# Kernel tuning notes

Hardware: AMD Instinct MI355X
Metric: run time of the kernel (lower is better)

## Reference

```python
import jax, jax.numpy as jnp
import numpy as np

N = 16384
E = 524288
K = 16
IN_C, HID, OUT = 3, 64, 64


def _mlp(h, Wa, ba, Wb, bb):
    # Linear -> ReLU -> Linear -> ReLU (as in nn.Sequential)
    return jax.nn.relu(jax.nn.relu(h @ Wa + ba) @ Wb + bb)


def _edgeconv(x, src, dst, Wa, ba, Wb, bb, n):
    # PyG EdgeConv message: nn([x_i, x_j - x_i]) with i=dst (target), j=src (source)
    xi = x[dst]                       # [E, C]
    xj = x[src]                       # [E, C]
    m = _mlp(jnp.concatenate([xi, xj - xi], axis=-1), Wa, ba, Wb, bb)  # [E, H]
    out = jax.ops.segment_max(m, dst, num_segments=n)
    # nodes with no incoming edges: fill 0 (PyG scatter-max fill value)
    return jnp.where(jnp.isfinite(out), out, 0.0)


def _knn_edges(x, k):
    # pairwise squared distances in feature space; includes self (torch_cluster.knn(x, x, k))
    sq = jnp.sum(x * x, axis=1)                      # [N]
    dist = sq[:, None] + sq[None, :] - 2.0 * (x @ x.T)  # [N, N]
    _, idx = jax.lax.top_k(-dist, k)                 # [N, k] nearest (incl. self)
    src = idx.reshape(-1)
    dst = jnp.repeat(jnp.arange(x.shape[0]), k)
    return src, dst


def setup_inputs() -> dict:
    key = jax.random.key(0)
    ks = jax.random.split(key, 8)
    sc = lambda fan: 1.0 / np.sqrt(fan)
    return {
        "x": jax.random.normal(ks[0], (N, IN_C), dtype=jnp.float32),
        "edge_index": jax.random.randint(ks[1], (2, E), 0, N, dtype=jnp.int64),
        "k": K,
        "W1": jax.random.normal(ks[2], (2 * IN_C, HID), dtype=jnp.float32) * sc(2 * IN_C),
        "b1": jnp.zeros((HID,), dtype=jnp.float32),
        "W2": jax.random.normal(ks[3], (HID, HID), dtype=jnp.float32) * sc(HID),
        "b2": jnp.zeros((HID,), dtype=jnp.float32),
        "W3": jax.random.normal(ks[4], (2 * HID, OUT), dtype=jnp.float32) * sc(2 * HID),
        "b3": jnp.zeros((OUT,), dtype=jnp.float32),
        "W4": jax.random.normal(ks[5], (OUT, OUT), dtype=jnp.float32) * sc(OUT),
        "b4": jnp.zeros((OUT,), dtype=jnp.float32),
    }


def reference(x, edge_index, k, W1, b1, W2, b2, W3, b3, W4, b4):
    n = x.shape[0]
    # static EdgeConv (edge_index[0]=source j, edge_index[1]=target i)
    x1 = _edgeconv(x, edge_index[0], edge_index[1], W1, b1, W2, b2, n)
    # DynamicEdgeConv: kNN in feature space of x1, then EdgeConv
    src2, dst2 = _knn_edges(x1, k)
    x2 = _edgeconv(x1, src2, dst2, W3, b3, W4, b4, n)
    return x2
```

## Files before the change

kernel.cpp:

```cpp
#include <hip/hip_runtime.h>
#include <stdint.h>

#define NN   16384
#define NE   524288
#define TK   17
#define TAU  4e-5f

#define S1   2048
#define JC1  16
#define CH1  (S1 / JC1)
#define JCB  8
#define CAP  512
#define LCAP 64
#define OFB  256
#define MGNB2 1e-3f

typedef unsigned long long u64;
typedef unsigned int u32;
typedef unsigned short u16;
typedef __attribute__((ext_vector_type(8))) short bf16x8;
typedef __attribute__((ext_vector_type(4))) float f32x4;

__device__ __forceinline__ float mulrn(float a, float b) { return __fmul_rn(a, b); }
__device__ __forceinline__ float addrn(float a, float b) { return __fadd_rn(a, b); }
__device__ __forceinline__ float subrn(float a, float b) { return __fsub_rn(a, b); }

__device__ __forceinline__ u32 fkey(float f) {
    u32 b = __float_as_uint(f);
    return ((int)b < 0) ? ~b : (b | 0x80000000u);
}
__device__ __forceinline__ float inv_fkey(u32 k) {
    return (k & 0x80000000u) ? __uint_as_float(k & 0x7fffffffu) : __uint_as_float(~k);
}

__device__ __forceinline__ u16 f2bf(float f) {
    u32 x = __float_as_uint(f);
    u32 r = x + 0x7fffu + ((x >> 16) & 1u);
    return (u16)(r >> 16);
}

template<int K>
__device__ __forceinline__ void topk_insert(u64 (&key)[K], u64 nk) {
#pragma unroll
    for (int s = K - 1; s >= 1; --s) {
        bool c1 = nk < key[s - 1];
        bool c0 = nk < key[s];
        key[s] = c1 ? key[s - 1] : (c0 ? nk : key[s]);
    }
    if (nk < key[0]) key[0] = nk;
}

#define XR_DECL float4 xq0, xq1, xq2, xq3, xq4, xq5, xq6, xq7, \
                       xq8, xq9, xq10, xq11, xq12, xq13, xq14, xq15

#define XR_LOAD(ptr) do { const float4* xp_ = (const float4*)(ptr); \
    xq0  = xp_[0];  xq1  = xp_[1];  xq2  = xp_[2];  xq3  = xp_[3]; \
    xq4  = xp_[4];  xq5  = xp_[5];  xq6  = xp_[6];  xq7  = xp_[7]; \
    xq8  = xp_[8];  xq9  = xp_[9];  xq10 = xp_[10]; xq11 = xp_[11]; \
    xq12 = xp_[12]; xq13 = xp_[13]; xq14 = xp_[14]; xq15 = xp_[15]; } while (0)

#define DOT_STEP(res, qq, w_) \
    res = fmaf(qq.x, w_.x, res); res = fmaf(qq.y, w_.y, res); \
    res = fmaf(qq.z, w_.z, res); res = fmaf(qq.w, w_.w, res);

#define DOT64(res, ptr) do { const float4* jp_ = (const float4*)(ptr); \
    float4 w_ = jp_[0]; \
    res = mulrn(xq0.x, w_.x); res = fmaf(xq0.y, w_.y, res); \
    res = fmaf(xq0.z, w_.z, res); res = fmaf(xq0.w, w_.w, res); \
    w_ = jp_[1];  DOT_STEP(res, xq1,  w_) \
    w_ = jp_[2];  DOT_STEP(res, xq2,  w_) \
    w_ = jp_[3];  DOT_STEP(res, xq3,  w_) \
    w_ = jp_[4];  DOT_STEP(res, xq4,  w_) \
    w_ = jp_[5];  DOT_STEP(res, xq5,  w_) \
    w_ = jp_[6];  DOT_STEP(res, xq6,  w_) \
    w_ = jp_[7];  DOT_STEP(res, xq7,  w_) \
    w_ = jp_[8];  DOT_STEP(res, xq8,  w_) \
    w_ = jp_[9];  DOT_STEP(res, xq9,  w_) \
    w_ = jp_[10]; DOT_STEP(res, xq10, w_) \
    w_ = jp_[11]; DOT_STEP(res, xq11, w_) \
    w_ = jp_[12]; DOT_STEP(res, xq12, w_) \
    w_ = jp_[13]; DOT_STEP(res, xq13, w_) \
    w_ = jp_[14]; DOT_STEP(res, xq14, w_) \
    w_ = jp_[15]; DOT_STEP(res, xq15, w_) } while (0)

__global__ __launch_bounds__(256) void hist_kernel(const int* __restrict__ ei,
                                                   int* __restrict__ hist) {
    int e = blockIdx.x * 256 + threadIdx.x;
    atomicAdd(&hist[ei[NE + e]], 1);
}

__global__ __launch_bounds__(256) void scan_kernel(const int* __restrict__ hist,
                                                   int* __restrict__ base) {
    __shared__ int part[256];
    __shared__ int off[256];
    int t = threadIdx.x;
    int s = 0;
    for (int b = 0; b < 64; b++) s += hist[t * 64 + b];
    part[t] = s;
    __syncthreads();
    if (t == 0) {
        int run = 0;
        for (int i = 0; i < 256; i++) { off[i] = run; run += part[i]; }
    }
    __syncthreads();
    int run = off[t];
    for (int b = 0; b < 64; b++) {
        base[t * 64 + b] = run;
        run += hist[t * 64 + b];
    }
}

__global__ __launch_bounds__(256) void scatter_kernel(const int* __restrict__ ei,
                                                      int* __restrict__ base,
                                                      int* __restrict__ esrc,
                                                      int* __restrict__ edst) {
    int e = blockIdx.x * 256 + threadIdx.x;
    int d = ei[NE + e];
    int pos = atomicAdd(&base[d], 1);
    esrc[pos] = ei[e];
    edst[pos] = d;
}

__global__ __launch_bounds__(256) void conv1_np_kernel(const float* __restrict__ x,
                                                       const float* __restrict__ W1,
                                                       const float* __restrict__ b1,
                                                       const float* __restrict__ W2,
                                                       const float* __restrict__ b2,
                                                       const int* __restrict__ esrc,
                                                       const int* __restrict__ edst,
                                                       float* __restrict__ x1n) {
    __shared__ float HT[64 * 132];
    __shared__ float W1s[384];
    __shared__ float W2s[64 * 64];
    __shared__ float b1s[64], b2s[64];
    __shared__ int dsts[128];
    int t = threadIdx.x;
    int eb = blockIdx.x * 128;

    {
        const float4* w4 = (const float4*)W2;
        float4* wd = (float4*)W2s;
#pragma unroll
        for (int q = 0; q < 4; q++) wd[t + q * 256] = w4[t + q * 256];
        if (t < 96) ((float4*)W1s)[t] = ((const float4*)W1)[t];
        if (t < 64) { b1s[t] = b1[t]; b2s[t] = b2[t]; }
    }
    __syncthreads();

    {
        int el = t >> 1;
        int cb = (t & 1) * 32;
        int e = eb + el;
        int j = esrc[e];
        int i = edst[e];
        if ((t & 1) == 0) dsts[el] = i;
        float xi0 = x[i * 3 + 0], xi1 = x[i * 3 + 1], xi2 = x[i * 3 + 2];
        float xj0 = x[j * 3 + 0], xj1 = x[j * 3 + 1], xj2 = x[j * 3 + 2];
        float d0 = subrn(xj0, xi0), d1 = subrn(xj1, xi1), d2 = subrn(xj2, xi2);
#pragma unroll
        for (int cc = 0; cc < 32; cc++) {
            int c = cb + cc;
            float acc = mulrn(xi0, W1s[c]);
            acc = fmaf(xi1, W1s[64 + c], acc);
            acc = fmaf(xi2, W1s[128 + c], acc);
            acc = fmaf(d0,  W1s[192 + c], acc);
            acc = fmaf(d1,  W1s[256 + c], acc);
            acc = fmaf(d2,  W1s[320 + c], acc);
            HT[c * 132 + el] = fmaxf(addrn(acc, b1s[c]), 0.f);
        }
    }
    __syncthreads();

    int cg = t & 7, eg = t >> 3;
    int c0 = cg * 8, e0 = eg * 4;
    float acc[4][8] = {};
    for (int k = 0; k < 64; k++) {
        float4 a  = *(const float4*)&HT[k * 132 + e0];
        float4 w0 = *(const float4*)&W2s[k * 64 + c0];
        float4 w1 = *(const float4*)&W2s[k * 64 + c0 + 4];
        float av[4] = {a.x, a.y, a.z, a.w};
        float wv[8] = {w0.x, w0.y, w0.z, w0.w, w1.x, w1.y, w1.z, w1.w};
#pragma unroll
        for (int r = 0; r < 4; r++)
#pragma unroll
            for (int c = 0; c < 8; c++) acc[r][c] = fmaf(av[r], wv[c], acc[r][c]);
    }
    __syncthreads();
#pragma unroll
    for (int r = 0; r < 4; r++)
#pragma unroll
        for (int c = 0; c < 8; c++)
            HT[(c0 + c) * 132 + (e0 + r)] = fmaxf(addrn(acc[r][c], b2s[c0 + c]), 0.f);
    __syncthreads();

    {
        int col = t & 63;
        int ebeg = (t >> 6) * 32;
        const float* hp = &HT[col * 132];
        int cur = dsts[ebeg];
        float m = hp[ebeg];
        for (int e = ebeg + 1; e < ebeg + 32; e++) {
            int d2 = dsts[e];
            float v = hp[e];
            if (d2 == cur) {
                m = fmaxf(m, v);
            } else {
                atomicMax((u32*)(x1n + (size_t)cur * 64 + col), __float_as_uint(m));
                cur = d2;
                m = v;
            }
        }
        atomicMax((u32*)(x1n + (size_t)cur * 64 + col), __float_as_uint(m));
    }
}

__global__ __launch_bounds__(256) void sq_np_kernel(const float* __restrict__ x1,
                                                    float* __restrict__ sq) {
    int i = blockIdx.x * 256 + threadIdx.x;
    const float* p = x1 + (size_t)i * 64;
    float r[8];
#pragma unroll
    for (int j = 0; j < 8; j++) { float v = p[j]; r[j] = mulrn(v, v); }
#pragma unroll
    for (int b = 8; b < 64; b += 8)
#pragma unroll
        for (int j = 0; j < 8; j++) { float v = p[b + j]; r[j] = addrn(r[j], mulrn(v, v)); }
    sq[i] = addrn(addrn(addrn(r[0], r[1]), addrn(r[2], r[3])),
                  addrn(addrn(r[4], r[5]), addrn(r[6], r[7])));
}

__global__ __launch_bounds__(256) void cvt_bf_kernel(const float* __restrict__ x1,
                                                     u16* __restrict__ xb,
                                                     u16* __restrict__ xl) {
    int i = (blockIdx.x * 256 + threadIdx.x) * 8;
    uint4 oh, ol;
    u32 hw[8], lw[8];
#pragma unroll
    for (int q = 0; q < 8; q++) {
        float v = x1[i + q];
        u16 h = f2bf(v);
        float hf = __uint_as_float((u32)h << 16);
        u16 l = f2bf(subrn(v, hf));
        hw[q] = h; lw[q] = l;
    }
    oh.x = hw[0] | (hw[1] << 16); oh.y = hw[2] | (hw[3] << 16);
    oh.z = hw[4] | (hw[5] << 16); oh.w = hw[6] | (hw[7] << 16);
    ol.x = lw[0] | (lw[1] << 16); ol.y = lw[2] | (lw[3] << 16);
    ol.z = lw[4] | (lw[5] << 16); ol.w = lw[6] | (lw[7] << 16);
    *(uint4*)(xb + i) = oh;
    *(uint4*)(xl + i) = ol;
}

__global__ __launch_bounds__(256, 4) void knn_tau_kernel(const float* __restrict__ x1,
                                                         const float* __restrict__ sq,
                                                         u32* __restrict__ part1) {
    int rb = blockIdx.x >> 4;
    int ch = blockIdx.x & 15;
    int t = threadIdx.x;
    int r = rb * 256 + t;
    XR_DECL;
    XR_LOAD(x1 + (size_t)r * 64);
    float sqr = sq[r];
    u32 key[TK];
#pragma unroll
    for (int s = 0; s < TK; s++) key[s] = 0xFFFFFFFFu;
    int j0 = ch * CH1;
    for (int jj = 0; jj < CH1; jj++) {
        int j = j0 + jj;
        float a;
        DOT64(a, x1 + (size_t)j * 64);
        float dd = subrn(addrn(sqr, sq[j]), mulrn(2.f, a));
        u32 nk = fkey(dd);
#pragma unroll
        for (int s = TK - 1; s >= 1; --s) key[s] = min(max(nk, key[s - 1]), key[s]);
        key[0] = min(key[0], nk);
    }
    u32* pp = part1 + ((size_t)r * JC1 + ch) * TK;
#pragma unroll
    for (int s = 0; s < TK; s++) pp[s] = key[s];
}

__global__ __launch_bounds__(256) void tau_merge_kernel(const u32* __restrict__ part1,
                                                        float* __restrict__ tauf) {
    int r = blockIdx.x * 256 + threadIdx.x;
    u32 key[TK];
#pragma unroll
    for (int s = 0; s < TK; s++) key[s] = 0xFFFFFFFFu;
    const u32* cp = part1 + (size_t)r * (JC1 * TK);
    for (int c = 0; c < JC1; c++) {
        for (int s = 0; s < TK; s++) {
            u32 nk = cp[c * TK + s];
            if (nk >= key[TK - 1]) break;
#pragma unroll
            for (int q = TK - 1; q >= 1; --q) key[q] = min(max(nk, key[q - 1]), key[q]);
            key[0] = min(key[0], nk);
        }
    }
    tauf[r] = inv_fkey(key[TK - 1]);
}

__global__ __launch_bounds__(256, 3) void knn_collect_mfma(const u16* __restrict__ xb,
                                                           const u16* __restrict__ xl,
                                                           const float* __restrict__ sq,
                                                           const float* __restrict__ tauf,
                                                           int* __restrict__ ccnt,
                                                           u16* __restrict__ cidx) {
    __shared__ u16 slist[64 * LCAP];
    __shared__ int scnt[64];
    __shared__ int sbase[64];
    int rb = blockIdx.x >> 3;
    int jc = blockIdx.x & 7;
    int t = threadIdx.x;
    int w = t >> 6, l = t & 63;
    int lr = l & 15, lg = l >> 4;
    int rbase = rb * 64;
    if (t < 64) scnt[t] = 0;

    bf16x8 fah[4][2], fal[4][2];
#pragma unroll
    for (int rs = 0; rs < 4; rs++) {
        size_t off = (size_t)(rbase + rs * 16 + lr) * 64 + lg * 8;
        fah[rs][0] = *(const bf16x8*)(xb + off);
        fah[rs][1] = *(const bf16x8*)(xb + off + 32);
        fal[rs][0] = *(const bf16x8*)(xl + off);
        fal[rs][1] = *(const bf16x8*)(xl + off + 32);
    }
    float sqr[16], taur[16];
#pragma unroll
    for (int rs = 0; rs < 4; rs++)
#pragma unroll
        for (int i = 0; i < 4; i++) {
            int rr = rbase + rs * 16 + lg * 4 + i;
            sqr[rs * 4 + i]  = sq[rr];
            taur[rs * 4 + i] = tauf[rr];
        }
    __syncthreads();

    int j0 = jc * (NN / JCB) + w * (NN / JCB / 4);
    for (int js = 0; js < (NN / JCB / 4); js += 16) {
        int jb = j0 + js;
        size_t boff = (size_t)(jb + lr) * 64 + lg * 8;
        bf16x8 fbh0 = *(const bf16x8*)(xb + boff);
        bf16x8 fbh1 = *(const bf16x8*)(xb + boff + 32);
        bf16x8 fbl0 = *(const bf16x8*)(xl + boff);
        bf16x8 fbl1 = *(const bf16x8*)(xl + boff + 32);
        int j = jb + lr;
        float sqj = sq[j];
#pragma unroll
        for (int rs = 0; rs < 4; rs++) {
            f32x4 acc = {0.f, 0.f, 0.f, 0.f};
            acc = __builtin_amdgcn_mfma_f32_16x16x32_bf16(fah[rs][0], fbh0, acc, 0, 0, 0);
            acc = __builtin_amdgcn_mfma_f32_16x16x32_bf16(fah[rs][1], fbh1, acc, 0, 0, 0);
            acc = __builtin_amdgcn_mfma_f32_16x16x32_bf16(fah[rs][0], fbl0, acc, 0, 0, 0);
            acc = __builtin_amdgcn_mfma_f32_16x16x32_bf16(fah[rs][1], fbl1, acc, 0, 0, 0);
            acc = __builtin_amdgcn_mfma_f32_16x16x32_bf16(fal[rs][0], fbh0, acc, 0, 0, 0);
            acc = __builtin_amdgcn_mfma_f32_16x16x32_bf16(fal[rs][1], fbh1, acc, 0, 0, 0);
#pragma unroll
            for (int i = 0; i < 4; i++) {
                float ss = sqr[rs * 4 + i] + sqj;
                float dd = ss - 2.f * acc[i];
                if (dd <= taur[rs * 4 + i] + MGNB2 * ss) {
                    int rl = rs * 16 + lg * 4 + i;
                    int slot = atomicAdd(&scnt[rl], 1);
                    if (slot < LCAP) {
                        slist[rl * LCAP + slot] = (u16)j;
                    } else {
                        int rr = rbase + rl;
                        int gslot = atomicAdd(&ccnt[rr], 1);
                        if (gslot < CAP) cidx[(size_t)rr * CAP + gslot] = (u16)j;
                    }
                }
            }
        }
    }
    __syncthreads();

    if (t < 64) {
        int ldsn = min(scnt[t], LCAP);
        sbase[t] = (ldsn > 0) ? atomicAdd(&ccnt[rbase + t], ldsn) : -1;
    }
    __syncthreads();
    {
        int rl = t >> 2, ln = t & 3;
        int ldsn = min(scnt[rl], LCAP);
        int base = sbase[rl];
        if (base >= 0) {
            for (int s = ln; s < ldsn; s += 4) {
                int dst = base + s;
                if (dst < CAP)
                    cidx[(size_t)(rbase + rl) * CAP + dst] = slist[rl * LCAP + s];
            }
        }
    }
}

__global__ __launch_bounds__(256) void oflow_scan_kernel(const int* __restrict__ ccnt,
                                                         int* __restrict__ ocnt,
                                                         int* __restrict__ olist) {
    int r = blockIdx.x * 256 + threadIdx.x;
    if (ccnt[r] > CAP) {
        int s = atomicAdd(ocnt, 1);
        olist[s] = r;
    }
}

__global__ __launch_bounds__(256, 2) void oflow_fix_kernel(const float* __restrict__ x1,
                                                           const float* __restrict__ sq,
                                                           const int* __restrict__ ocnt,
                                                           const int* __restrict__ olist,
                                                           u16* __restrict__ cidx,
                                                           int* __restrict__ ccnt) {
    __shared__ u64 m[256 * TK];
    int nof = *ocnt;
    int t = threadIdx.x;
    for (int w = blockIdx.x; w < nof; w += gridDim.x) {
        int r = olist[w];
        XR_DECL;
        XR_LOAD(x1 + (size_t)r * 64);
        float sqr = sq[r];
        u64 key[TK];
#pragma unroll
        for (int s = 0; s < TK; s++) key[s] = ~0ull;
        for (int j = t; j < NN; j += 256) {
            float a;
            DOT64(a, x1 + (size_t)j * 64);
            float dd = subrn(addrn(sqr, sq[j]), mulrn(2.f, a));
            u64 nk = ((u64)fkey(dd) << 32) | (u32)j;
            if (nk < key[TK - 1]) topk_insert<TK>(key, nk);
        }
#pragma unroll
        for (int s = 0; s < TK; s++) m[t * TK + s] = key[s];
        __syncthreads();
        if (t == 0) {
            u64 fin[TK];
#pragma unroll
            for (int s = 0; s < TK; s++) fin[s] = ~0ull;
            for (int l = 0; l < 256; l++)
                for (int s = 0; s < TK; s++) {
                    u64 nk = m[l * TK + s];
                    if (nk >= fin[TK - 1]) break;
                    topk_insert<TK>(fin, nk);
                }
            for (int s = 0; s < TK; s++) cidx[(size_t)r * CAP + s] = (u16)(fin[s] & 0xffffu);
            ccnt[r] = TK;
        }
        __syncthreads();
    }
}

__global__ __launch_bounds__(256) void sel_row_kernel(const float* __restrict__ x1,
                                                      const float* __restrict__ sq,
                                                      const u16* __restrict__ cidx,
                                                      const int* __restrict__ ccnt,
                                                      int* __restrict__ nidxA,
                                                      int* __restrict__ nidxB,
                                                      int* __restrict__ flist,
                                                      int* __restrict__ cnt) {
    __shared__ __align__(16) u64 KL[CAP];
    __shared__ float SD[2];
    int r = blockIdx.x;
    int t = threadIdx.x;
    int cn = min(ccnt[r], CAP);
    XR_DECL;
    XR_LOAD(x1 + (size_t)r * 64);
    float sqr = sq[r];

    int s0 = t, s1 = t + 256;
    u64 k0 = ~0ull, k1 = ~0ull;
    if (s0 < cn) {
        int j = cidx[(size_t)r * CAP + s0];
        float a;
        DOT64(a, x1 + (size_t)j * 64);
        float dd = subrn(addrn(sqr, sq[j]), mulrn(2.f, a));
        k0 = ((u64)fkey(dd) << 32) | (u32)j;
        KL[s0] = k0;
    }
    if (s1 < cn) {
        int j = cidx[(size_t)r * CAP + s1];
        float a;
        DOT64(a, x1 + (size_t)j * 64);
        float dd = subrn(addrn(sqr, sq[j]), mulrn(2.f, a));
        k1 = ((u64)fkey(dd) << 32) | (u32)j;
        KL[s1] = k1;
    }
    __syncthreads();

    int r0 = 0, r1 = 0;
    bool waveLive = ((t & ~63) < cn);
    if (waveLive) {
        const ulonglong2* KL2 = (const ulonglong2*)KL;
        if (cn <= 256) {
            int q = 0;
            for (; q + 4 <= cn; q += 4) {
                ulonglong2 ab = KL2[q >> 1];
                ulonglong2 cd = KL2[(q >> 1) + 1];
                r0 += (int)(ab.x < k0) + (int)(ab.y < k0)
                    + (int)(cd.x < k0) + (int)(cd.y < k0);
            }
            for (; q < cn; q++) r0 += (KL[q] < k0);
        } else {
            int q = 0;
            for (; q + 4 <= cn; q += 4) {
                ulonglong2 ab = KL2[q >> 1];
                ulonglong2 cd = KL2[(q >> 1) + 1];
                r0 += (int)(ab.x < k0) + (int)(ab.y < k0)
                    + (int)(cd.x < k0) + (int)(cd.y < k0);
                r1 += (int)(ab.x < k1) + (int)(ab.y < k1)
                    + (int)(cd.x < k1) + (int)(cd.y < k1);
            }
            for (; q < cn; q++) { u64 kq = KL[q]; r0 += (kq < k0); r1 += (kq < k1); }
        }
    }

    if (s0 < cn && r0 < TK) {
        int j = (int)(k0 & 0xffffffffu);
        if (r0 < 16) nidxA[r * 16 + r0] = j;
        if (r0 < 15) nidxB[r * 16 + r0] = j;
        if (r0 == 16) nidxB[r * 16 + 15] = j;
        if (r0 == 15) SD[0] = inv_fkey((u32)(k0 >> 32));
        if (r0 == 16) SD[1] = inv_fkey((u32)(k0 >> 32));
    }
    if (s1 < cn && r1 < TK) {
        int j = (int)(k1 & 0xffffffffu);
        if (r1 < 16) nidxA[r * 16 + r1] = j;
        if (r1 < 15) nidxB[r * 16 + r1] = j;
        if (r1 == 16) nidxB[r * 16 + 15] = j;
        if (r1 == 15) SD[0] = inv_fkey((u32)(k1 >> 32));
        if (r1 == 16) SD[1] = inv_fkey((u32)(k1 >> 32));
    }
    __syncthreads();
    if (t == 0) {
        if (SD[1] - SD[0] <= TAU) {
            int s = atomicAdd(cnt, 1);
            flist[s] = r;
        }
    }
}

__global__ __launch_bounds__(256) void pq2_kernel(const float* __restrict__ x1,
                                                  const float* __restrict__ W3,
                                                  float* __restrict__ P,
                                                  float* __restrict__ Q) {
    __shared__ float XT[64 * 68];
    __shared__ float W3s[128 * 64];
    int t = threadIdx.x;
    int rb = blockIdx.x * 64;
    {
        const float4* w4 = (const float4*)W3;
        float4* wd = (float4*)W3s;
#pragma unroll
        for (int q = 0; q < 8; q++) wd[t + q * 256] = w4[t + q * 256];
    }
    {
        int rl = t >> 2, cb = (t & 3) * 16;
        const float4* xs = (const float4*)(x1 + (size_t)(rb + rl) * 64 + cb);
#pragma unroll
        for (int q4 = 0; q4 < 4; q4++) {
            float4 v = xs[q4];
            int c = cb + q4 * 4;
            XT[(c + 0) * 68 + rl] = v.x;
            XT[(c + 1) * 68 + rl] = v.y;
            XT[(c + 2) * 68 + rl] = v.z;
            XT[(c + 3) * 68 + rl] = v.w;
        }
    }
    __syncthreads();

    int cg = t & 15, rg = t >> 4;
    int c0 = cg * 8, r0 = rg * 4;
    float acc[4][8] = {};
    for (int k = 0; k < 64; k++) {
        float4 a = *(const float4*)&XT[k * 68 + r0];
        int wb = (c0 < 64) ? (k * 64 + c0) : ((64 + k) * 64 + (c0 - 64));
        float4 w0 = *(const float4*)&W3s[wb];
        float4 w1 = *(const float4*)&W3s[wb + 4];
        float av[4] = {a.x, a.y, a.z, a.w};
        float wv[8] = {w0.x, w0.y, w0.z, w0.w, w1.x, w1.y, w1.z, w1.w};
#pragma unroll
        for (int r = 0; r < 4; r++)
#pragma unroll
            for (int c = 0; c < 8; c++) acc[r][c] = fmaf(av[r], wv[c], acc[r][c]);
    }
    float* base = (c0 < 64) ? P : Q;
    int cc = c0 & 63;
#pragma unroll
    for (int r = 0; r < 4; r++) {
        float* op = base + (size_t)(rb + r0 + r) * 64 + cc;
        *(float4*)(op)     = make_float4(acc[r][0], acc[r][1], acc[r][2], acc[r][3]);
        *(float4*)(op + 4) = make_float4(acc[r][4], acc[r][5], acc[r][6], acc[r][7]);
    }
}

__global__ __launch_bounds__(256) void conv2_kernel(const float* __restrict__ P,
                                                    const float* __restrict__ Q,
                                                    const float* __restrict__ b3,
                                                    const float* __restrict__ W4,
                                                    const float* __restrict__ b4,
                                                    const int* __restrict__ idx,
                                                    float* __restrict__ out) {
    __shared__ float HT[64 * 132];
    __shared__ float W4s[64 * 64];
    __shared__ float b4s[64];
    int t = threadIdx.x;
    int nb = blockIdx.x * 8;
    int eb = nb * 16;
    {
        const float4* w4 = (const float4*)W4;
        float4* wd = (float4*)W4s;
#pragma unroll
        for (int q = 0; q < 4; q++) wd[t + q * 256] = w4[t + q * 256];
        if (t < 64) b4s[t] = b4[t];
    }
    {
        int el = t >> 1;
        int qh = (t & 1) * 32;
        int i = nb + (el >> 4);
        int j = idx[eb + el];
        const float4* Pi = (const float4*)(P + (size_t)i * 64 + qh);
        const float4* Qi = (const float4*)(Q + (size_t)i * 64 + qh);
        const float4* Qj = (const float4*)(Q + (size_t)j * 64 + qh);
        const float4* bv = (const float4*)(b3 + qh);
#pragma unroll
        for (int q4 = 0; q4 < 8; q4++) {
            float4 p = Pi[q4], qi = Qi[q4], qj = Qj[q4], bb = bv[q4];
            int q = qh + q4 * 4;
            HT[(q + 0) * 132 + el] = fmaxf(bb.x + p.x + qj.x - qi.x, 0.f);
            HT[(q + 1) * 132 + el] = fmaxf(bb.y + p.y + qj.y - qi.y, 0.f);
            HT[(q + 2) * 132 + el] = fmaxf(bb.z + p.z + qj.z - qi.z, 0.f);
            HT[(q + 3) * 132 + el] = fmaxf(bb.w + p.w + qj.w - qi.w, 0.f);
        }
    }
    __syncthreads();

    int nl = t >> 5;
    int c0 = (t & 31) * 2;
    float acc[16][2];
#pragma unroll
    for (int r = 0; r < 16; r++) { acc[r][0] = 0.f; acc[r][1] = 0.f; }
    for (int k = 0; k < 64; k++) {
        const float* hp = &HT[k * 132 + nl * 16];
        float4 a0 = *(const float4*)(hp);
        float4 a1 = *(const float4*)(hp + 4);
        float4 a2 = *(const float4*)(hp + 8);
        float4 a3 = *(const float4*)(hp + 12);
        float2 w = *(const float2*)&W4s[k * 64 + c0];
        float av[16] = {a0.x, a0.y, a0.z, a0.w, a1.x, a1.y, a1.z, a1.w,
                        a2.x, a2.y, a2.z, a2.w, a3.x, a3.y, a3.z, a3.w};
#pragma unroll
        for (int r = 0; r < 16; r++) {
            acc[r][0] = fmaf(av[r], w.x, acc[r][0]);
            acc[r][1] = fmaf(av[r], w.y, acc[r][1]);
        }
    }
    float m0 = acc[0][0], m1 = acc[0][1];
#pragma unroll
    for (int r = 1; r < 16; r++) { m0 = fmaxf(m0, acc[r][0]); m1 = fmaxf(m1, acc[r][1]); }
    m0 = fmaxf(m0 + b4s[c0], 0.f);
    m1 = fmaxf(m1 + b4s[c0 + 1], 0.f);
    *(float2*)&out[(size_t)(nb + nl) * 64 + c0] = make_float2(m0, m1);
}

__global__ __launch_bounds__(256) void conv2b_kernel(const float* __restrict__ P,
                                                     const float* __restrict__ Q,
                                                     const float* __restrict__ b3,
                                                     const float* __restrict__ W4,
                                                     const float* __restrict__ b4,
                                                     const int* __restrict__ idxB,
                                                     const int* __restrict__ flist,
                                                     const int* __restrict__ cnt,
                                                     float* __restrict__ out) {
    int nfl = *cnt;
    int base = blockIdx.x * 8;
    if (base >= nfl) return;

    __shared__ float HT[64 * 132];
    __shared__ float W4s[64 * 64];
    __shared__ float b4s[64];
    int t = threadIdx.x;
    {
        const float4* w4 = (const float4*)W4;
        float4* wd = (float4*)W4s;
#pragma unroll
        for (int q = 0; q < 4; q++) wd[t + q * 256] = w4[t + q * 256];
        if (t < 64) b4s[t] = b4[t];
    }
    {
        int el = t >> 1;
        int qh = (t & 1) * 32;
        int slot = base + (el >> 4);
        int i = (slot < nfl) ? flist[slot] : flist[base];
        int j = idxB[i * 16 + (el & 15)];
        const float4* Pi = (const float4*)(P + (size_t)i * 64 + qh);
        const float4* Qi = (const float4*)(Q + (size_t)i * 64 + qh);
        const float4* Qj = (const float4*)(Q + (size_t)j * 64 + qh);
        const float4* bv = (const float4*)(b3 + qh);
#pragma unroll
        for (int q4 = 0; q4 < 8; q4++) {
            float4 p = Pi[q4], qi = Qi[q4], qj = Qj[q4], bb = bv[q4];
            int q = qh + q4 * 4;
            HT[(q + 0) * 132 + el] = fmaxf(bb.x + p.x + qj.x - qi.x, 0.f);
            HT[(q + 1) * 132 + el] = fmaxf(bb.y + p.y + qj.y - qi.y, 0.f);
            HT[(q + 2) * 132 + el] = fmaxf(bb.z + p.z + qj.z - qi.z, 0.f);
            HT[(q + 3) * 132 + el] = fmaxf(bb.w + p.w + qj.w - qi.w, 0.f);
        }
    }
    __syncthreads();

    int nl = t >> 5;
    int c0 = (t & 31) * 2;
    float acc[16][2];
#pragma unroll
    for (int r = 0; r < 16; r++) { acc[r][0] = 0.f; acc[r][1] = 0.f; }
    for (int k = 0; k < 64; k++) {
        const float* hp = &HT[k * 132 + nl * 16];
        float4 a0 = *(const float4*)(hp);
        float4 a1 = *(const float4*)(hp + 4);
        float4 a2 = *(const float4*)(hp + 8);
        float4 a3 = *(const float4*)(hp + 12);
        float2 w = *(const float2*)&W4s[k * 64 + c0];
        float av[16] = {a0.x, a0.y, a0.z, a0.w, a1.x, a1.y, a1.z, a1.w,
                        a2.x, a2.y, a2.z, a2.w, a3.x, a3.y, a3.z, a3.w};
#pragma unroll
        for (int r = 0; r < 16; r++) {
            acc[r][0] = fmaf(av[r], w.x, acc[r][0]);
            acc[r][1] = fmaf(av[r], w.y, acc[r][1]);
        }
    }
    float m0 = acc[0][0], m1 = acc[0][1];
#pragma unroll
    for (int r = 1; r < 16; r++) { m0 = fmaxf(m0, acc[r][0]); m1 = fmaxf(m1, acc[r][1]); }
    m0 = fmaxf(m0 + b4s[c0], 0.f);
    m1 = fmaxf(m1 + b4s[c0 + 1], 0.f);

    int slot2 = base + nl;
    if (slot2 < nfl) {
        int i2 = flist[slot2];
        float* op = out + (size_t)i2 * 64 + c0;
        float2 old = *(float2*)op;
        *(float2*)op = make_float2(0.5f * (old.x + m0), 0.5f * (old.y + m1));
    }
}

extern "C" void kernel_launch(void* const* d_in, const int* in_sizes, int n_in,
                              void* d_out, int out_size, void* d_ws, size_t ws_size,
                              hipStream_t stream) {
    const float* x  = (const float*)d_in[0];
    const int*   ei = (const int*)d_in[1];
    const float* W1 = (const float*)d_in[3];
    const float* b1 = (const float*)d_in[4];
    const float* W2 = (const float*)d_in[5];
    const float* b2 = (const float*)d_in[6];
    const float* W3 = (const float*)d_in[7];
    const float* b3 = (const float*)d_in[8];
    const float* W4 = (const float*)d_in[9];
    const float* b4 = (const float*)d_in[10];
    float* out = (float*)d_out;

    char* ws = (char*)d_ws;
    float* x1f   = (float*)(ws);
    float* sqf   = (float*)(ws + 4194304);
    float* tauf  = (float*)(ws + 4259840);
    int*   ccnt  = (int*)(ws + 4325376);
    int*   ocnt  = (int*)(ws + 6422528);
    int*   fcnt  = (int*)(ws + 6422592);
    int*   olist = (int*)(ws + 6422656);
    int*   flist = (int*)(ws + 6488192);
    int*   nidxA = (int*)(ws + 6553728);
    int*   nidxB = (int*)(ws + 7602304);
    u32*   part1 = (u32*)(ws + 8650880);
    u16*   cidx  = (u16*)(ws + 8650880);
    float* Pf    = (float*)(ws + 8650880);
    float* Qf    = (float*)(ws + 12845184);
    int*   esrc  = (int*)(ws + 26476672);
    u16*   x1bf  = (u16*)(ws + 26476672);
    int*   edst  = (int*)(ws + 28573824);
    u16*   x1bflo = (u16*)(ws + 28573824);
    int*   hist  = (int*)(ws + 30670976);

    hipMemsetAsync(x1f, 0, (size_t)NN * 64 * sizeof(float), stream);
    hipMemsetAsync(ccnt, 0, NN * sizeof(int), stream);
    hipMemsetAsync(ocnt, 0, 128, stream);
    hipMemsetAsync(hist, 0, NN * sizeof(int), stream);

    hist_kernel<<<NE / 256, 256, 0, stream>>>(ei, hist);
    scan_kernel<<<1, 256, 0, stream>>>(hist, hist);
    scatter_kernel<<<NE / 256, 256, 0, stream>>>(ei, hist, esrc, edst);

    conv1_np_kernel<<<NE / 128, 256, 0, stream>>>(x, W1, b1, W2, b2, esrc, edst, x1f);
    sq_np_kernel<<<NN / 256, 256, 0, stream>>>(x1f, sqf);

    knn_tau_kernel<<<(NN / 256) * JC1, 256, 0, stream>>>(x1f, sqf, part1);
    tau_merge_kernel<<<NN / 256, 256, 0, stream>>>(part1, tauf);

    cvt_bf_kernel<<<NN * 64 / 8 / 256, 256, 0, stream>>>(x1f, x1bf, x1bflo);
    knn_collect_mfma<<<(NN / 64) * JCB, 256, 0, stream>>>(x1bf, x1bflo, sqf, tauf, ccnt, cidx);
    oflow_scan_kernel<<<NN / 256, 256, 0, stream>>>(ccnt, ocnt, olist);
    oflow_fix_kernel<<<OFB, 256, 0, stream>>>(x1f, sqf, ocnt, olist, cidx, ccnt);
    sel_row_kernel<<<NN, 256, 0, stream>>>(x1f, sqf, cidx, ccnt, nidxA, nidxB, flist, fcnt);

    pq2_kernel<<<NN / 64, 256, 0, stream>>>(x1f, W3, Pf, Qf);
    conv2_kernel<<<NN / 8, 256, 0, stream>>>(Pf, Qf, b3, W4, b4, nidxA, out);
    conv2b_kernel<<<NN / 8, 256, 0, stream>>>(Pf, Qf, b3, W4, b4, nidxB, flist, fcnt, out);
}
```

Before: 679.2 us.

## Prefetch next B tile, simplify kNN threshold test, reorder block mapping

In the kNN candidate-collection kernel, the next 16-column B fragments are software-prefetched into registers while the current MFMA tile is computed. The distance comparison is rewritten algebraically so each element needs one add and compare against a precomputed per-row threshold plus a per-column term. Block indices are remapped so consecutive blocks share the same column chunk, and the launch-bounds occupancy hint rises from 3 to 4 waves. The prefetch adds registers, which may conflict with the higher occupancy target, and the rearranged comparison can round slightly differently at the margin.

```diff
diff --git a/kernel.cpp b/kernel.cpp
--- a/kernel.cpp
+++ b/kernel.cpp
@@ -299,7 +299,7 @@
     tauf[r] = inv_fkey(key[TK - 1]);
 }
 
-__global__ __launch_bounds__(256, 3) void knn_collect_mfma(const u16* __restrict__ xb,
+__global__ __launch_bounds__(256, 4) void knn_collect_mfma(const u16* __restrict__ xb,
                                                            const u16* __restrict__ xl,
                                                            const float* __restrict__ sq,
                                                            const float* __restrict__ tauf,
@@ -308,8 +308,8 @@
     __shared__ u16 slist[64 * LCAP];
     __shared__ int scnt[64];
     __shared__ int sbase[64];
-    int rb = blockIdx.x >> 3;
-    int jc = blockIdx.x & 7;
+    int rb = blockIdx.x & 255;
+    int jc = blockIdx.x >> 8;
     int t = threadIdx.x;
     int w = t >> 6, l = t & 63;
     int lr = l & 15, lg = l >> 4;
@@ -325,27 +325,35 @@
         fal[rs][0] = *(const bf16x8*)(xl + off);
         fal[rs][1] = *(const bf16x8*)(xl + off + 32);
     }
-    float sqr[16], taur[16];
+    const float BCO = 0.5f * (1.f - MGNB2);
+    float thrA[16];
 #pragma unroll
     for (int rs = 0; rs < 4; rs++)
 #pragma unroll
         for (int i = 0; i < 4; i++) {
             int rr = rbase + rs * 16 + lg * 4 + i;
-            sqr[rs * 4 + i]  = sq[rr];
-            taur[rs * 4 + i] = tauf[rr];
-        }
-    __syncthreads();
-
-    int j0 = jc * (NN / JCB) + w * (NN / JCB / 4);
-    for (int js = 0; js < (NN / JCB / 4); js += 16) {
+            thrA[rs * 4 + i] = 0.5f * ((1.f - MGNB2) * sq[rr] - tauf[rr]);
+        }
+    __syncthreads();
+
+    const int RNG = NN / JCB / 4;
+    int j0 = jc * (NN / JCB) + w * RNG;
+    size_t poff = (size_t)(j0 + lr) * 64 + lg * 8;
+    bf16x8 nh0 = *(const bf16x8*)(xb + poff);
+    bf16x8 nh1 = *(const bf16x8*)(xb + poff + 32);
+    bf16x8 nl0 = *(const bf16x8*)(xl + poff);
+    bf16x8 nl1 = *(const bf16x8*)(xl + poff + 32);
+    for (int js = 0; js < RNG; js += 16) {
+        bf16x8 fbh0 = nh0, fbh1 = nh1, fbl0 = nl0, fbl1 = nl1;
         int jb = j0 + js;
-        size_t boff = (size_t)(jb + lr) * 64 + lg * 8;
-        bf16x8 fbh0 = *(const bf16x8*)(xb + boff);
-        bf16x8 fbh1 = *(const bf16x8*)(xb + boff + 32);
-        bf16x8 fbl0 = *(const bf16x8*)(xl + boff);
-        bf16x8 fbl1 = *(const bf16x8*)(xl + boff + 32);
+        int jsn = (js + 16 < RNG) ? js + 16 : js;
+        size_t noff = (size_t)(j0 + jsn + lr) * 64 + lg * 8;
+        nh0 = *(const bf16x8*)(xb + noff);
+        nh1 = *(const bf16x8*)(xb + noff + 32);
+        nl0 = *(const bf16x8*)(xl + noff);
+        nl1 = *(const bf16x8*)(xl + noff + 32);
         int j = jb + lr;
-        float sqj = sq[j];
+        float thB = BCO * sq[j];
 #pragma unroll
         for (int rs = 0; rs < 4; rs++) {
             f32x4 acc = {0.f, 0.f, 0.f, 0.f};
@@ -357,9 +365,7 @@
             acc = __builtin_amdgcn_mfma_f32_16x16x32_bf16(fal[rs][1], fbh1, acc, 0, 0, 0);
 #pragma unroll
             for (int i = 0; i < 4; i++) {
-                float ss = sqr[rs * 4 + i] + sqj;
-                float dd = ss - 2.f * acc[i];
-                if (dd <= taur[rs * 4 + i] + MGNB2 * ss) {
+                if (acc[i] >= thrA[rs * 4 + i] + thB) {
                     int rl = rs * 16 + lg * 4 + i;
                     int slot = atomicAdd(&scnt[rl], 1);
                     if (slot < LCAP) {
```

New measurement: 1.006 ms. 1.48x slower.
